# Performance work log

Measured on AMD Instinct MI355X. Metric: run time of the kernel, lower is better.

Reference implementation:

```python
import jax, jax.numpy as jnp
import numpy as np

NEG = -1e30

def setup_inputs() -> dict:
    key = jax.random.key(0)
    ks = jax.random.split(key, 11)
    B, NA, NB = 8, 2048, 2048
    in_A, in_B, out_dim = 256, 256, 64
    s = 0.05
    return {
        "h_A": jax.random.normal(ks[0], (B, NA, in_A), jnp.float32),
        "h_B": jax.random.normal(ks[1], (B, NB, in_B), jnp.float32),
        "mask": jax.random.bernoulli(ks[2], 0.5, (B, NA, NB)),
        "WA_w": jax.random.normal(ks[3], (in_A, out_dim), jnp.float32) * s,
        "WA_b": jax.random.normal(ks[4], (out_dim,), jnp.float32) * s,
        "WB_w": jax.random.normal(ks[5], (in_B, out_dim), jnp.float32) * s,
        "WB_b": jax.random.normal(ks[6], (out_dim,), jnp.float32) * s,
        "aA_w": jax.random.normal(ks[7], (out_dim,), jnp.float32) * s,
        "aA_b": jax.random.normal(ks[8], (), jnp.float32) * s,
        "aB_w": jax.random.normal(ks[9], (out_dim,), jnp.float32) * s,
        "aB_b": jax.random.normal(ks[10], (), jnp.float32) * s,
    }

def reference(h_A, h_B, mask, WA_w, WA_b, WB_w, WB_b, aA_w, aA_b, aB_w, aB_b):
    # Linear projections: z_A [B,NA,D], z_B [B,NB,D]
    z_A = jnp.einsum('bnd,df->bnf', h_A, WA_w) + WA_b
    z_B = jnp.einsum('bmd,df->bmf', h_B, WB_w) + WB_b
    # Additive attention scores: [B,NA,1] + [B,1,NB] -> [B,NA,NB]
    sA = z_A @ aA_w + aA_b  # [B,NA]
    sB = z_B @ aB_w + aB_b  # [B,NB]
    e = sA[:, :, None] + sB[:, None, :]
    e = jnp.where(mask, e, NEG)
    e = jax.nn.leaky_relu(e, negative_slope=0.01)
    alpha = jax.nn.softmax(e, axis=-1)
    alpha = jnp.where(mask, alpha, 0.0)
    # Weighted sum over neighbors
    return jnp.einsum('bnm,bmf->bnf', alpha, z_B)
```

## Files before the change

kernel.cpp:

```cpp
#include <hip/hip_runtime.h>

typedef short bf16x8 __attribute__((ext_vector_type(8)));
typedef float f32x4 __attribute__((ext_vector_type(4)));

__device__ __forceinline__ unsigned short f2bf(float x) {
  unsigned u = __float_as_uint(x);
  u += 0x7FFFu + ((u >> 16) & 1u);
  return (unsigned short)(u >> 16);
}
__device__ __forceinline__ float bf2f(unsigned short h) {
  return __uint_as_float(((unsigned)h) << 16);
}

__global__ __launch_bounds__(256) void zb_kernel(
    const float* __restrict__ hB, const float* __restrict__ WB_w,
    const float* __restrict__ WB_b, const float* __restrict__ aB_w,
    const float* __restrict__ aB_b,
    unsigned short* __restrict__ zBT, float* __restrict__ sB,
    float* __restrict__ msB_blk) {
  __shared__ char wt[32768];
  __shared__ char hl[16384];
  __shared__ float redp[4][16];
  __shared__ float sred[32];

  const int t = threadIdx.x, w = t >> 6, l = t & 63;
  const int q = l >> 4, ln = l & 15;
  const int m0g = blockIdx.x * 32;
  const int b = m0g >> 11, mloc = m0g & 2047;

  {
    const int f = t >> 2, kseg = t & 3;
    #pragma unroll
    for (int j = 0; j < 8; ++j) {
      const int k0 = kseg * 64 + j * 8;
      bf16x8 v;
      #pragma unroll
      for (int jj = 0; jj < 8; ++jj)
        v[jj] = (short)f2bf(WB_w[(k0 + jj) * 64 + f]);
      *(bf16x8*)(wt + ((f * 512 + k0 * 2) ^ ((f & 7) << 4))) = v;
    }
  }
  {
    #pragma unroll
    for (int i = 0; i < 8; ++i) {
      const int idx = i * 1024 + t * 4;
      const int row = idx >> 8, k = idx & 255;
      const float4 x = *(const float4*)(hB + (size_t)m0g * 256 + idx);
      uint2 pk;
      pk.x = (unsigned)f2bf(x.x) | ((unsigned)f2bf(x.y) << 16);
      pk.y = (unsigned)f2bf(x.z) | ((unsigned)f2bf(x.w) << 16);
      *(uint2*)(hl + ((row * 512 + k * 2) ^ ((row & 7) << 4))) = pk;
    }
  }
  __syncthreads();
  const int rt = w & 1, fpair = w >> 1;
  f32x4 acc[2];
  acc[0] = (f32x4){0.f, 0.f, 0.f, 0.f};
  acc[1] = acc[0];
  const int rowA = rt * 16 + ln;
  #pragma unroll
  for (int kk = 0; kk < 8; ++kk) {
    const int ko = kk * 64 + q * 16;
    const bf16x8 a = *(const bf16x8*)(hl + ((rowA * 512 + ko) ^ ((rowA & 7) << 4)));
    #pragma unroll
    for (int j = 0; j < 2; ++j) {
      const int f = fpair * 32 + j * 16 + ln;
      const bf16x8 bb = *(const bf16x8*)(wt + ((f * 512 + ko) ^ ((f & 7) << 4)));
      acc[j] = __builtin_amdgcn_mfma_f32_16x16x32_bf16(a, bb, acc[j], 0, 0, 0);
    }
  }
  float z[2][4];
  float p[4] = {0.f, 0.f, 0.f, 0.f};
  #pragma unroll
  for (int j = 0; j < 2; ++j) {
    const int f = fpair * 32 + j * 16 + ln;
    const float bias = WB_b[f], aw = aB_w[f];
    #pragma unroll
    for (int r = 0; r < 4; ++r) {
      const float zz = acc[j][r] + bias;
      z[j][r] = zz;
      p[r] += zz * aw;
    }
  }
  #pragma unroll
  for (int r = 0; r < 4; ++r) {
    #pragma unroll
    for (int off = 1; off < 16; off <<= 1) p[r] += __shfl_xor(p[r], off, 16);
  }
  if (ln == 0) {
    #pragma unroll
    for (int r = 0; r < 4; ++r) redp[w][q * 4 + r] = p[r];
  }
  __syncthreads();
  char* zt = hl;
  #pragma unroll
  for (int j = 0; j < 2; ++j) {
    const int f = fpair * 32 + j * 16 + ln;
    uint2 pk;
    pk.x = (unsigned)f2bf(z[j][0]) | ((unsigned)f2bf(z[j][1]) << 16);
    pk.y = (unsigned)f2bf(z[j][2]) | ((unsigned)f2bf(z[j][3]) << 16);
    *(uint2*)(zt + f * 80 + (rt * 16 + q * 4) * 2) = pk;
  }
  if (t < 32) {
    const int rtm = t >> 4, mi = t & 15;
    const float s = redp[rtm][mi] + redp[rtm + 2][mi] + aB_b[0];
    sB[m0g + t] = s;
    sred[t] = s;
  }
  __syncthreads();
  if (t == 0) {
    float bm = sred[0];
    #pragma unroll
    for (int i = 1; i < 32; ++i) bm = fmaxf(bm, sred[i]);
    msB_blk[blockIdx.x] = bm;
  }
  {
    const int f = t >> 2, mseg = t & 3;
    const bf16x8 v = *(const bf16x8*)(zt + f * 80 + mseg * 16);
    *(bf16x8*)(zBT + (size_t)b * 131072 + f * 2048 + mloc + mseg * 8) = v;
  }
}

struct Pref {
  bf16x8 za, zb2;
  uint2 mk;
  int4 m32a, m32b;
};

__device__ __forceinline__ void gat_load(Pref& p,
    const unsigned short* zrow, const unsigned char* mk8, const int* mk32,
    const bool use8, const int m0) {
  p.za = *(const bf16x8*)(zrow + m0);
  p.zb2 = *(const bf16x8*)(zrow + m0 + 8);
  if (use8) {
    p.mk = *(const uint2*)(mk8 + m0);
  } else {
    p.m32a = *(const int4*)(mk32 + m0);
    p.m32b = *(const int4*)(mk32 + m0 + 4);
  }
}

__device__ __forceinline__ void gat_body(const Pref& p, char* zc, char* wc,
    const float* sBl, const int m0, const int m8, const float sAr, const float M,
    const bool use8, const int zw0, const int zw1, const int wbyte, float& ds) {
  *(bf16x8*)(zc + zw0) = p.za;
  *(bf16x8*)(zc + zw1) = p.zb2;
  const int sbase = m0 + m8 * 8;
  const float4 s0 = *(const float4*)(sBl + sbase);
  const float4 s1 = *(const float4*)(sBl + sbase + 4);
  const float sbx[8] = {s0.x, s0.y, s0.z, s0.w, s1.x, s1.y, s1.z, s1.w};
  int km[8];
  if (use8) {
    #pragma unroll
    for (int j = 0; j < 4; ++j) {
      km[j] = (p.mk.x >> (8 * j)) & 0xFF;
      km[j + 4] = (p.mk.y >> (8 * j)) & 0xFF;
    }
  } else {
    km[0] = p.m32a.x; km[1] = p.m32a.y; km[2] = p.m32a.z; km[3] = p.m32a.w;
    km[4] = p.m32b.x; km[5] = p.m32b.y; km[6] = p.m32b.z; km[7] = p.m32b.w;
  }
  unsigned short wb[8];
  #pragma unroll
  for (int j = 0; j < 8; ++j) {
    const float x = sAr + sbx[j];
    const float e = x >= 0.f ? x : 0.01f * x;
    const float v = km[j] ? __expf(e - M) : 0.f;
    wb[j] = f2bf(v);
    ds += bf2f(wb[j]);
  }
  uint4 pk;
  pk.x = (unsigned)wb[0] | ((unsigned)wb[1] << 16);
  pk.y = (unsigned)wb[2] | ((unsigned)wb[3] << 16);
  pk.z = (unsigned)wb[4] | ((unsigned)wb[5] << 16);
  pk.w = (unsigned)wb[6] | ((unsigned)wb[7] << 16);
  *(uint4*)(wc + wbyte) = pk;
}

__device__ __forceinline__ void gat_mfma(const char* zc, const char* wc,
    f32x4& acc, const int fb, const int ar, const int q) {
  #pragma unroll
  for (int kk = 0; kk < 4; ++kk) {
    const int ko = kk * 64 + q * 16;
    const bf16x8 bb = *(const bf16x8*)(zc + ((fb * 256 + ko) ^ ((fb & 7) << 4)));
    const bf16x8 aa = *(const bf16x8*)(wc + ((ar * 256 + ko) ^ ((ar & 7) << 4)));
    acc = __builtin_amdgcn_mfma_f32_16x16x32_bf16(aa, bb, acc, 0, 0, 0);
  }
}

__global__ __launch_bounds__(512, 4) void gat_kernel(
    const unsigned short* __restrict__ zBT, const float* __restrict__ hA,
    const float* __restrict__ WA_w, const float* __restrict__ WA_b,
    const float* __restrict__ aA_w, const float* __restrict__ aA_b,
    const float* __restrict__ sB, const float* __restrict__ msB_blk,
    const unsigned char* __restrict__ mask8, const int* __restrict__ mask32,
    float* __restrict__ out) {
  const int b = blockIdx.y, n0 = blockIdx.x * 32;
  const int t = threadIdx.x, w = t >> 6, l = t & 63;
  const int q = l >> 4, ln = l & 15;

  __shared__ char zbl0[16384], zbl1[16384];
  __shared__ char wl0[8192], wl1[8192];
  __shared__ float sBl[2048];
  __shared__ float vAl[256];
  __shared__ float sAl[32];
  __shared__ float dl[32];
  __shared__ float cAl;
  __shared__ unsigned dfl[4];

  if (t < 256) {
    const unsigned vdet = mask8[t * 4 + 1];
    const unsigned long long bal = __ballot(vdet != 0);
    if (l == 0) dfl[w] = (bal != 0ull) ? 1u : 0u;
    const float4* wr = (const float4*)(WA_w + t * 64);
    const float4* a4 = (const float4*)aA_w;
    float s = 0.f;
    #pragma unroll
    for (int i = 0; i < 16; ++i) {
      const float4 x = wr[i], y = a4[i];
      s += x.x * y.x + x.y * y.y + x.z * y.z + x.w * y.w;
    }
    vAl[t] = s;
  } else {
    const int u = t - 256;
    ((float4*)sBl)[u * 2] = ((const float4*)(sB + b * 2048))[u * 2];
    ((float4*)sBl)[u * 2 + 1] = ((const float4*)(sB + b * 2048))[u * 2 + 1];
    if (u == 0) {
      float ca = aA_b[0];
      for (int f = 0; f < 64; ++f) ca += WA_b[f] * aA_w[f];
      cAl = ca;
    }
  }
  float mb = msB_blk[b * 64 + l];
  #pragma unroll
  for (int off = 1; off < 64; off <<= 1) mb = fmaxf(mb, __shfl_xor(mb, off, 64));
  __syncthreads();
  const bool use8 = (dfl[0] | dfl[1] | dfl[2] | dfl[3]) != 0;
  {
    const float4 vA4 = ((const float4*)vAl)[l];
    const float cA0 = cAl;
    #pragma unroll
    for (int rr = 0; rr < 4; ++rr) {
      const int row = w * 4 + rr;
      const float4 h4 = *(const float4*)(hA + ((size_t)(b * 2048 + n0 + row)) * 256 + l * 4);
      float s = h4.x * vA4.x + h4.y * vA4.y + h4.z * vA4.z + h4.w * vA4.w;
      #pragma unroll
      for (int off = 1; off < 64; off <<= 1) s += __shfl_xor(s, off, 64);
      if (l == 0) sAl[row] = s + cA0;
    }
  }
  __syncthreads();

  const int r = t >> 4, m8 = t & 15;
  const float sAr = sAl[r];
  const float Mf = sAr + mb;
  const float M = Mf >= 0.f ? Mf : 0.01f * Mf;
  float ds = 0.f;
  f32x4 acc = (f32x4){0.f, 0.f, 0.f, 0.f};

  const int zf = t >> 3, zseg = t & 7;
  const unsigned short* zrow = zBT + (size_t)b * 131072 + zf * 2048 + zseg * 16;
  const size_t mrowe = ((size_t)(b * 2048 + n0 + r)) * 2048 + m8 * 8;
  const unsigned char* mk8 = mask8 + mrowe;
  const int* mk32 = mask32 + mrowe;
  const int zbase = zf * 256 + zseg * 32;
  const int swz = (zf & 7) << 4;
  const int zw0 = zbase ^ swz, zw1 = (zbase + 16) ^ swz;
  const int wbyte = (r * 256 + m8 * 16) ^ ((r & 7) << 4);
  const int fb = (w >> 1) * 16 + ln;
  const int ar = (w & 1) * 16 + ln;

  Pref pA, pB;
  gat_load(pA, zrow, mk8, mk32, use8, 0);
  for (int mt = 0; mt < 16; mt += 2) {
    gat_load(pB, zrow, mk8, mk32, use8, (mt + 1) * 128);
    gat_body(pA, zbl0, wl0, sBl, mt * 128, m8, sAr, M, use8, zw0, zw1, wbyte, ds);
    __syncthreads();
    gat_mfma(zbl0, wl0, acc, fb, ar, q);
    gat_load(pA, zrow, mk8, mk32, use8, ((mt + 2) & 15) * 128);
    gat_body(pB, zbl1, wl1, sBl, (mt + 1) * 128, m8, sAr, M, use8, zw0, zw1, wbyte, ds);
    __syncthreads();
    gat_mfma(zbl1, wl1, acc, fb, ar, q);
  }
  #pragma unroll
  for (int off = 1; off < 16; off <<= 1) ds += __shfl_xor(ds, off, 16);
  if (m8 == 0) dl[r] = ds;
  __syncthreads();
  #pragma unroll
  for (int rr = 0; rr < 4; ++rr) {
    const int n = (w & 1) * 16 + q * 4 + rr;
    const float d = dl[n];
    out[((size_t)(b * 2048 + n0 + n)) * 64 + fb] = d > 0.f ? acc[rr] / d : 0.f;
  }
}

extern "C" void kernel_launch(void* const* d_in, const int* in_sizes, int n_in,
                              void* d_out, int out_size, void* d_ws, size_t ws_size,
                              hipStream_t stream) {
  const float* h_A = (const float*)d_in[0];
  const float* h_B = (const float*)d_in[1];
  const unsigned char* mask8 = (const unsigned char*)d_in[2];
  const int* mask32 = (const int*)d_in[2];
  const float* WA_w = (const float*)d_in[3];
  const float* WA_b = (const float*)d_in[4];
  const float* WB_w = (const float*)d_in[5];
  const float* WB_b = (const float*)d_in[6];
  const float* aA_w = (const float*)d_in[7];
  const float* aA_b = (const float*)d_in[8];
  const float* aB_w = (const float*)d_in[9];
  const float* aB_b = (const float*)d_in[10];
  float* out = (float*)d_out;

  char* wsb = (char*)d_ws;
  unsigned short* zBT = (unsigned short*)wsb;
  float* sB      = (float*)(wsb + 2097152);
  float* msB_blk = (float*)(wsb + 2162688);

  zb_kernel<<<512, 256, 0, stream>>>(h_B, WB_w, WB_b, aB_w, aB_b, zBT, sB, msB_blk);
  gat_kernel<<<dim3(64, 8), 512, 0, stream>>>(zBT, h_A, WA_w, WA_b, aA_w, aA_b,
                                              sB, msB_blk, mask8, mask32, out);
}
```

Measured before the change: 59.30 us.

## Double rows per block and switch to 32x32x16 MFMA with split-K merge

Each block now handles 64 query rows instead of 32, so every staged zB tile in shared memory is reused by twice as many rows, halving zB reloads. The matmul moves from 16x16x32 to 32x32x16 MFMA, with the two wave halves splitting K and merging partial sums through shared memory at the end. The int32 mask path is packed into bytes at load time. Cost: grid drops to 256 blocks (one wave on a 256-CU part), and each thread does twice the exp work and holds more registers, so occupancy and latency hiding may suffer.

```diff
diff --git a/kernel.cpp b/kernel.cpp
--- a/kernel.cpp
+++ b/kernel.cpp
@@ -2,6 +2,7 @@
 
 typedef short bf16x8 __attribute__((ext_vector_type(8)));
 typedef float f32x4 __attribute__((ext_vector_type(4)));
+typedef float f32x16 __attribute__((ext_vector_type(16)));
 
 __device__ __forceinline__ unsigned short f2bf(float x) {
   unsigned u = __float_as_uint(x);
@@ -123,68 +124,80 @@
 
 struct Pref {
   bf16x8 za, zb2;
-  uint2 mk;
-  int4 m32a, m32b;
+  uint2 mk0, mk1;
 };
 
-__device__ __forceinline__ void gat_load(Pref& p,
-    const unsigned short* zrow, const unsigned char* mk8, const int* mk32,
-    const bool use8, const int m0) {
+__device__ __forceinline__ uint2 pack_mask32(const int* p) {
+  const int4 a = *(const int4*)p;
+  const int4 c = *(const int4*)(p + 4);
+  uint2 r;
+  r.x = (a.x ? 1u : 0u) | (a.y ? 0x100u : 0u) | (a.z ? 0x10000u : 0u) | (a.w ? 0x1000000u : 0u);
+  r.y = (c.x ? 1u : 0u) | (c.y ? 0x100u : 0u) | (c.z ? 0x10000u : 0u) | (c.w ? 0x1000000u : 0u);
+  return r;
+}
+
+__device__ __forceinline__ void gat_load(Pref& p, const unsigned short* zrow,
+    const unsigned char* mk8a, const unsigned char* mk8b,
+    const int* mk32a, const int* mk32b, const bool use8, const int m0) {
   p.za = *(const bf16x8*)(zrow + m0);
   p.zb2 = *(const bf16x8*)(zrow + m0 + 8);
   if (use8) {
-    p.mk = *(const uint2*)(mk8 + m0);
+    p.mk0 = *(const uint2*)(mk8a + m0);
+    p.mk1 = *(const uint2*)(mk8b + m0);
   } else {
-    p.m32a = *(const int4*)(mk32 + m0);
-    p.m32b = *(const int4*)(mk32 + m0 + 4);
+    p.mk0 = pack_mask32(mk32a + m0);
+    p.mk1 = pack_mask32(mk32b + m0);
   }
 }
 
 __device__ __forceinline__ void gat_body(const Pref& p, char* zc, char* wc,
-    const float* sBl, const int m0, const int m8, const float sAr, const float M,
-    const bool use8, const int zw0, const int zw1, const int wbyte, float& ds) {
+    const float* sBl, const int m0, const int m8,
+    const float sA0, const float sA1, const float M0, const float M1,
+    const int zw0, const int zw1, const int wbyte0, float& ds0, float& ds1) {
   *(bf16x8*)(zc + zw0) = p.za;
   *(bf16x8*)(zc + zw1) = p.zb2;
   const int sbase = m0 + m8 * 8;
   const float4 s0 = *(const float4*)(sBl + sbase);
   const float4 s1 = *(const float4*)(sBl + sbase + 4);
   const float sbx[8] = {s0.x, s0.y, s0.z, s0.w, s1.x, s1.y, s1.z, s1.w};
-  int km[8];
-  if (use8) {
-    #pragma unroll
-    for (int j = 0; j < 4; ++j) {
-      km[j] = (p.mk.x >> (8 * j)) & 0xFF;
-      km[j + 4] = (p.mk.y >> (8 * j)) & 0xFF;
-    }
-  } else {
-    km[0] = p.m32a.x; km[1] = p.m32a.y; km[2] = p.m32a.z; km[3] = p.m32a.w;
-    km[4] = p.m32b.x; km[5] = p.m32b.y; km[6] = p.m32b.z; km[7] = p.m32b.w;
-  }
-  unsigned short wb[8];
+  unsigned km0[8], km1[8];
+  #pragma unroll
+  for (int j = 0; j < 4; ++j) {
+    km0[j] = (p.mk0.x >> (8 * j)) & 0xFFu; km0[j + 4] = (p.mk0.y >> (8 * j)) & 0xFFu;
+    km1[j] = (p.mk1.x >> (8 * j)) & 0xFFu; km1[j + 4] = (p.mk1.y >> (8 * j)) & 0xFFu;
+  }
+  unsigned short w0[8], w1[8];
   #pragma unroll
   for (int j = 0; j < 8; ++j) {
-    const float x = sAr + sbx[j];
-    const float e = x >= 0.f ? x : 0.01f * x;
-    const float v = km[j] ? __expf(e - M) : 0.f;
-    wb[j] = f2bf(v);
-    ds += bf2f(wb[j]);
-  }
-  uint4 pk;
-  pk.x = (unsigned)wb[0] | ((unsigned)wb[1] << 16);
-  pk.y = (unsigned)wb[2] | ((unsigned)wb[3] << 16);
-  pk.z = (unsigned)wb[4] | ((unsigned)wb[5] << 16);
-  pk.w = (unsigned)wb[6] | ((unsigned)wb[7] << 16);
-  *(uint4*)(wc + wbyte) = pk;
+    const float x0 = sA0 + sbx[j];
+    const float e0 = x0 >= 0.f ? x0 : 0.01f * x0;
+    const float v0 = km0[j] ? __expf(e0 - M0) : 0.f;
+    w0[j] = f2bf(v0); ds0 += bf2f(w0[j]);
+    const float x1 = sA1 + sbx[j];
+    const float e1 = x1 >= 0.f ? x1 : 0.01f * x1;
+    const float v1 = km1[j] ? __expf(e1 - M1) : 0.f;
+    w1[j] = f2bf(v1); ds1 += bf2f(w1[j]);
+  }
+  uint4 pk0, pk1;
+  pk0.x = (unsigned)w0[0] | ((unsigned)w0[1] << 16);
+  pk0.y = (unsigned)w0[2] | ((unsigned)w0[3] << 16);
+  pk0.z = (unsigned)w0[4] | ((unsigned)w0[5] << 16);
+  pk0.w = (unsigned)w0[6] | ((unsigned)w0[7] << 16);
+  pk1.x = (unsigned)w1[0] | ((unsigned)w1[1] << 16);
+  pk1.y = (unsigned)w1[2] | ((unsigned)w1[3] << 16);
+  pk1.z = (unsigned)w1[4] | ((unsigned)w1[5] << 16);
+  pk1.w = (unsigned)w1[6] | ((unsigned)w1[7] << 16);
+  *(uint4*)(wc + wbyte0) = pk0;
+  *(uint4*)(wc + wbyte0 + 8192) = pk1;
 }
 
 __device__ __forceinline__ void gat_mfma(const char* zc, const char* wc,
-    f32x4& acc, const int fb, const int ar, const int q) {
-  #pragma unroll
-  for (int kk = 0; kk < 4; ++kk) {
-    const int ko = kk * 64 + q * 16;
-    const bf16x8 bb = *(const bf16x8*)(zc + ((fb * 256 + ko) ^ ((fb & 7) << 4)));
-    const bf16x8 aa = *(const bf16x8*)(wc + ((ar * 256 + ko) ^ ((ar & 7) << 4)));
-    acc = __builtin_amdgcn_mfma_f32_16x16x32_bf16(aa, bb, acc, 0, 0, 0);
+    f32x16& acc, const int abase, const int aswz, const int bbase, const int bswz) {
+  #pragma unroll
+  for (int ks = 0; ks < 4; ++ks) {
+    const bf16x8 aa = *(const bf16x8*)(wc + ((abase + ks * 32) ^ aswz));
+    const bf16x8 bb = *(const bf16x8*)(zc + ((bbase + ks * 32) ^ bswz));
+    acc = __builtin_amdgcn_mfma_f32_32x32x16_bf16(aa, bb, acc, 0, 0, 0);
   }
 }
 
@@ -195,16 +208,15 @@
     const float* __restrict__ sB, const float* __restrict__ msB_blk,
     const unsigned char* __restrict__ mask8, const int* __restrict__ mask32,
     float* __restrict__ out) {
-  const int b = blockIdx.y, n0 = blockIdx.x * 32;
+  const int b = blockIdx.y, n0 = blockIdx.x * 64;
   const int t = threadIdx.x, w = t >> 6, l = t & 63;
-  const int q = l >> 4, ln = l & 15;
 
   __shared__ char zbl0[16384], zbl1[16384];
-  __shared__ char wl0[8192], wl1[8192];
+  __shared__ char wl0[16384], wl1[16384];
   __shared__ float sBl[2048];
   __shared__ float vAl[256];
-  __shared__ float sAl[32];
-  __shared__ float dl[32];
+  __shared__ float sAl[64];
+  __shared__ float dl[64];
   __shared__ float cAl;
   __shared__ unsigned dfl[4];
 
@@ -212,9 +224,9 @@
     const unsigned vdet = mask8[t * 4 + 1];
     const unsigned long long bal = __ballot(vdet != 0);
     if (l == 0) dfl[w] = (bal != 0ull) ? 1u : 0u;
+    float s = 0.f;
     const float4* wr = (const float4*)(WA_w + t * 64);
     const float4* a4 = (const float4*)aA_w;
-    float s = 0.f;
     #pragma unroll
     for (int i = 0; i < 16; ++i) {
       const float4 x = wr[i], y = a4[i];
@@ -240,8 +252,8 @@
     const float4 vA4 = ((const float4*)vAl)[l];
     const float cA0 = cAl;
     #pragma unroll
-    for (int rr = 0; rr < 4; ++rr) {
-      const int row = w * 4 + rr;
+    for (int rr = 0; rr < 8; ++rr) {
+      const int row = w * 8 + rr;
       const float4 h4 = *(const float4*)(hA + ((size_t)(b * 2048 + n0 + row)) * 256 + l * 4);
       float s = h4.x * vA4.x + h4.y * vA4.y + h4.z * vA4.z + h4.w * vA4.w;
       #pragma unroll
@@ -251,46 +263,75 @@
   }
   __syncthreads();
 
-  const int r = t >> 4, m8 = t & 15;
-  const float sAr = sAl[r];
-  const float Mf = sAr + mb;
-  const float M = Mf >= 0.f ? Mf : 0.01f * Mf;
-  float ds = 0.f;
-  f32x4 acc = (f32x4){0.f, 0.f, 0.f, 0.f};
+  const int r0 = t >> 4, m8 = t & 15;
+  const float sA0 = sAl[r0], sA1 = sAl[r0 + 32];
+  const float M0f = sA0 + mb, M1f = sA1 + mb;
+  const float M0 = M0f >= 0.f ? M0f : 0.01f * M0f;
+  const float M1 = M1f >= 0.f ? M1f : 0.01f * M1f;
+  float ds0 = 0.f, ds1 = 0.f;
+  f32x16 acc;
+  #pragma unroll
+  for (int i = 0; i < 16; ++i) acc[i] = 0.f;
 
   const int zf = t >> 3, zseg = t & 7;
   const unsigned short* zrow = zBT + (size_t)b * 131072 + zf * 2048 + zseg * 16;
-  const size_t mrowe = ((size_t)(b * 2048 + n0 + r)) * 2048 + m8 * 8;
-  const unsigned char* mk8 = mask8 + mrowe;
-  const int* mk32 = mask32 + mrowe;
-  const int zbase = zf * 256 + zseg * 32;
-  const int swz = (zf & 7) << 4;
-  const int zw0 = zbase ^ swz, zw1 = (zbase + 16) ^ swz;
-  const int wbyte = (r * 256 + m8 * 16) ^ ((r & 7) << 4);
-  const int fb = (w >> 1) * 16 + ln;
-  const int ar = (w & 1) * 16 + ln;
+  const int zswz = (zf & 15) << 4;
+  const int zw0 = (zf * 256 + zseg * 32) ^ zswz;
+  const int zw1 = (zf * 256 + zseg * 32 + 16) ^ zswz;
+  const size_t mrow0 = ((size_t)(b * 2048 + n0 + r0)) * 2048 + m8 * 8;
+  const size_t mrow1 = mrow0 + (size_t)32 * 2048;
+  const unsigned char* mk8a = mask8 + mrow0;
+  const unsigned char* mk8b = mask8 + mrow1;
+  const int* mk32a = mask32 + mrow0;
+  const int* mk32b = mask32 + mrow1;
+  const int wbyte0 = (r0 * 256 + m8 * 16) ^ ((r0 & 15) << 4);
+  const int wn = w & 1, wf = (w >> 1) & 1, wm = w >> 2;
+  const int arow = wn * 32 + (l & 31);
+  const int brow = wf * 32 + (l & 31);
+  const int abase = arow * 256 + wm * 128 + (l >> 5) * 16;
+  const int bbase = brow * 256 + wm * 128 + (l >> 5) * 16;
+  const int aswz = (arow & 15) << 4;
+  const int bswz = (brow & 15) << 4;
 
   Pref pA, pB;
-  gat_load(pA, zrow, mk8, mk32, use8, 0);
+  gat_load(pA, zrow, mk8a, mk8b, mk32a, mk32b, use8, 0);
   for (int mt = 0; mt < 16; mt += 2) {
-    gat_load(pB, zrow, mk8, mk32, use8, (mt + 1) * 128);
-    gat_body(pA, zbl0, wl0, sBl, mt * 128, m8, sAr, M, use8, zw0, zw1, wbyte, ds);
+    gat_load(pB, zrow, mk8a, mk8b, mk32a, mk32b, use8, (mt + 1) * 128);
+    gat_body(pA, zbl0, wl0, sBl, mt * 128, m8, sA0, sA1, M0, M1, zw0, zw1, wbyte0, ds0, ds1);
     __syncthreads();
-    gat_mfma(zbl0, wl0, acc, fb, ar, q);
-    gat_load(pA, zrow, mk8, mk32, use8, ((mt + 2) & 15) * 128);
-    gat_body(pB, zbl1, wl1, sBl, (mt + 1) * 128, m8, sAr, M, use8, zw0, zw1, wbyte, ds);
+    gat_mfma(zbl0, wl0, acc, abase, aswz, bbase, bswz);
+    gat_load(pA, zrow, mk8a, mk8b, mk32a, mk32b, use8, ((mt + 2) & 15) * 128);
+    gat_body(pB, zbl1, wl1, sBl, (mt + 1) * 128, m8, sA0, sA1, M0, M1, zw0, zw1, wbyte0, ds0, ds1);
     __syncthreads();
-    gat_mfma(zbl1, wl1, acc, fb, ar, q);
-  }
-  #pragma unroll
-  for (int off = 1; off < 16; off <<= 1) ds += __shfl_xor(ds, off, 16);
-  if (m8 == 0) dl[r] = ds;
-  __syncthreads();
-  #pragma unroll
-  for (int rr = 0; rr < 4; ++rr) {
-    const int n = (w & 1) * 16 + q * 4 + rr;
-    const float d = dl[n];
-    out[((size_t)(b * 2048 + n0 + n)) * 64 + fb] = d > 0.f ? acc[rr] / d : 0.f;
+    gat_mfma(zbl1, wl1, acc, abase, aswz, bbase, bswz);
+  }
+
+  #pragma unroll
+  for (int off = 1; off < 16; off <<= 1) {
+    ds0 += __shfl_xor(ds0, off, 16);
+    ds1 += __shfl_xor(ds1, off, 16);
+  }
+  if (m8 == 0) { dl[r0] = ds0; dl[r0 + 32] = ds1; }
+  __syncthreads();
+  float* mrg = (float*)zbl0;
+  const int quad = (wn * 2 + wf) * 1024;
+  if (wm == 1) {
+    #pragma unroll
+    for (int r = 0; r < 16; ++r) {
+      const int row = (r & 3) + 8 * (r >> 2) + 4 * (l >> 5);
+      mrg[quad + row * 32 + (l & 31)] = acc[r];
+    }
+  }
+  __syncthreads();
+  if (wm == 0) {
+    #pragma unroll
+    for (int r = 0; r < 16; ++r) {
+      const int row = (r & 3) + 8 * (r >> 2) + 4 * (l >> 5);
+      const float v = acc[r] + mrg[quad + row * 32 + (l & 31)];
+      const int n = wn * 32 + row;
+      const float d = dl[n];
+      out[((size_t)(b * 2048 + n0 + n)) * 64 + wf * 32 + (l & 31)] = d > 0.f ? v / d : 0.f;
+    }
   }
 }
 
@@ -317,6 +358,6 @@
   float* msB_blk = (float*)(wsb + 2162688);
 
   zb_kernel<<<512, 256, 0, stream>>>(h_B, WB_w, WB_b, aB_w, aB_b, zBT, sB, msB_blk);
-  gat_kernel<<<dim3(64, 8), 512, 0, stream>>>(zBT, h_A, WA_w, WA_b, aA_w, aA_b,
+  gat_kernel<<<dim3(32, 8), 512, 0, stream>>>(zBT, h_A, WA_w, WA_b, aA_w, aA_b,
                                               sB, msB_blk, mask8, mask32, out);
 }
```

After: 60.81 us. +2.5%, slower.

## Split attention over neighbor quarters, keep operands in registers, add merge kernel

Applied to the files above, without the earlier changes.

The attention kernel now splits the neighbor dimension into four chunks across a third grid axis and writes partial weighted sums and denominators, which a new merge kernel adds up and normalizes. The per-row sA projection moves into the zB kernel. The main loop feeds MFMAs directly from registers: weights are built in-register as the A operand and z_B is loaded straight from global memory as B operands, so the shared-memory staging and per-iteration barriers are gone. The cost is about 17 MB of extra partial-result traffic, a third kernel launch, and more redundant global z_B loads per block.

```diff
diff --git a/kernel.cpp b/kernel.cpp
--- a/kernel.cpp
+++ b/kernel.cpp
@@ -8,25 +8,55 @@
   u += 0x7FFFu + ((u >> 16) & 1u);
   return (unsigned short)(u >> 16);
 }
-__device__ __forceinline__ float bf2f(unsigned short h) {
-  return __uint_as_float(((unsigned)h) << 16);
-}
 
 __global__ __launch_bounds__(256) void zb_kernel(
     const float* __restrict__ hB, const float* __restrict__ WB_w,
     const float* __restrict__ WB_b, const float* __restrict__ aB_w,
     const float* __restrict__ aB_b,
+    const float* __restrict__ hA, const float* __restrict__ WA_w,
+    const float* __restrict__ WA_b, const float* __restrict__ aA_w,
+    const float* __restrict__ aA_b,
     unsigned short* __restrict__ zBT, float* __restrict__ sB,
-    float* __restrict__ msB_blk) {
+    float* __restrict__ msB_blk, float* __restrict__ sA) {
   __shared__ char wt[32768];
   __shared__ char hl[16384];
   __shared__ float redp[4][16];
   __shared__ float sred[32];
+  __shared__ float vAl[256];
+  __shared__ float cAl;
 
   const int t = threadIdx.x, w = t >> 6, l = t & 63;
   const int q = l >> 4, ln = l & 15;
   const int m0g = blockIdx.x * 32;
   const int b = m0g >> 11, mloc = m0g & 2047;
+
+  {
+    float sa = 0.f;
+    const float4* wr4 = (const float4*)(WA_w + t * 64);
+    const float4* aa4 = (const float4*)aA_w;
+    #pragma unroll
+    for (int i = 0; i < 16; ++i) {
+      const float4 x = wr4[i], y = aa4[i];
+      sa += x.x * y.x + x.y * y.y + x.z * y.z + x.w * y.w;
+    }
+    vAl[t] = sa;
+    if (t == 0) {
+      float ca = aA_b[0];
+      for (int f = 0; f < 64; ++f) ca += WA_b[f] * aA_w[f];
+      cAl = ca;
+    }
+    __syncthreads();
+    const float4 v4 = ((const float4*)vAl)[l];
+    #pragma unroll
+    for (int rr = 0; rr < 8; ++rr) {
+      const int row = w * 8 + rr;
+      const float4 h4 = *(const float4*)(hA + (size_t)(m0g + row) * 256 + l * 4);
+      float s = h4.x * v4.x + h4.y * v4.y + h4.z * v4.z + h4.w * v4.w;
+      #pragma unroll
+      for (int off = 1; off < 64; off <<= 1) s += __shfl_xor(s, off, 64);
+      if (l == 0) sA[m0g + row] = s + cAl;
+    }
+  }
 
   {
     const int f = t >> 2, kseg = t & 3;
@@ -122,176 +152,131 @@
 }
 
 struct Pref {
-  bf16x8 za, zb2;
   uint2 mk;
-  int4 m32a, m32b;
+  bf16x8 z0, z1, z2, z3;
 };
 
-__device__ __forceinline__ void gat_load(Pref& p,
-    const unsigned short* zrow, const unsigned char* mk8, const int* mk32,
-    const bool use8, const int m0) {
-  p.za = *(const bf16x8*)(zrow + m0);
-  p.zb2 = *(const bf16x8*)(zrow + m0 + 8);
-  if (use8) {
-    p.mk = *(const uint2*)(mk8 + m0);
-  } else {
-    p.m32a = *(const int4*)(mk32 + m0);
-    p.m32b = *(const int4*)(mk32 + m0 + 4);
-  }
-}
-
-__device__ __forceinline__ void gat_body(const Pref& p, char* zc, char* wc,
-    const float* sBl, const int m0, const int m8, const float sAr, const float M,
-    const bool use8, const int zw0, const int zw1, const int wbyte, float& ds) {
-  *(bf16x8*)(zc + zw0) = p.za;
-  *(bf16x8*)(zc + zw1) = p.zb2;
-  const int sbase = m0 + m8 * 8;
-  const float4 s0 = *(const float4*)(sBl + sbase);
-  const float4 s1 = *(const float4*)(sBl + sbase + 4);
-  const float sbx[8] = {s0.x, s0.y, s0.z, s0.w, s1.x, s1.y, s1.z, s1.w};
-  int km[8];
-  if (use8) {
-    #pragma unroll
-    for (int j = 0; j < 4; ++j) {
-      km[j] = (p.mk.x >> (8 * j)) & 0xFF;
-      km[j + 4] = (p.mk.y >> (8 * j)) & 0xFF;
-    }
-  } else {
-    km[0] = p.m32a.x; km[1] = p.m32a.y; km[2] = p.m32a.z; km[3] = p.m32a.w;
-    km[4] = p.m32b.x; km[5] = p.m32b.y; km[6] = p.m32b.z; km[7] = p.m32b.w;
-  }
-  unsigned short wb[8];
+__device__ __forceinline__ uint2 pack_mask32(const int* p) {
+  const int4 a = *(const int4*)p;
+  const int4 c = *(const int4*)(p + 4);
+  uint2 r;
+  r.x = (a.x ? 1u : 0u) | (a.y ? 0x100u : 0u) | (a.z ? 0x10000u : 0u) | (a.w ? 0x1000000u : 0u);
+  r.y = (c.x ? 1u : 0u) | (c.y ? 0x100u : 0u) | (c.z ? 0x10000u : 0u) | (c.w ? 0x1000000u : 0u);
+  return r;
+}
+
+__device__ __forceinline__ void gat_load(Pref& p, const unsigned char* mp8,
+    const int* mp32, const unsigned short* zp0, const unsigned short* zp1,
+    const unsigned short* zp2, const unsigned short* zp3,
+    const bool use8, const int c) {
+  const int m = (c & 15) * 32;
+  if (use8) p.mk = *(const uint2*)(mp8 + m);
+  else p.mk = pack_mask32(mp32 + m);
+  p.z0 = *(const bf16x8*)(zp0 + m);
+  p.z1 = *(const bf16x8*)(zp1 + m);
+  p.z2 = *(const bf16x8*)(zp2 + m);
+  p.z3 = *(const bf16x8*)(zp3 + m);
+}
+
+__device__ __forceinline__ void gat_compute(const Pref& p, const float* sBl,
+    const int c, const int lq8, const float sAr, const float M,
+    f32x4& a0, f32x4& a1, f32x4& a2, f32x4& a3, float& ds) {
+  const int sb0 = c * 32 + lq8;
+  const float4 s0 = *(const float4*)(sBl + sb0);
+  const float4 s1 = *(const float4*)(sBl + sb0 + 4);
+  const float sx[8] = {s0.x, s0.y, s0.z, s0.w, s1.x, s1.y, s1.z, s1.w};
+  bf16x8 af;
   #pragma unroll
   for (int j = 0; j < 8; ++j) {
-    const float x = sAr + sbx[j];
-    const float e = x >= 0.f ? x : 0.01f * x;
-    const float v = km[j] ? __expf(e - M) : 0.f;
-    wb[j] = f2bf(v);
-    ds += bf2f(wb[j]);
-  }
-  uint4 pk;
-  pk.x = (unsigned)wb[0] | ((unsigned)wb[1] << 16);
-  pk.y = (unsigned)wb[2] | ((unsigned)wb[3] << 16);
-  pk.z = (unsigned)wb[4] | ((unsigned)wb[5] << 16);
-  pk.w = (unsigned)wb[6] | ((unsigned)wb[7] << 16);
-  *(uint4*)(wc + wbyte) = pk;
-}
-
-__device__ __forceinline__ void gat_mfma(const char* zc, const char* wc,
-    f32x4& acc, const int fb, const int ar, const int q) {
-  #pragma unroll
-  for (int kk = 0; kk < 4; ++kk) {
-    const int ko = kk * 64 + q * 16;
-    const bf16x8 bb = *(const bf16x8*)(zc + ((fb * 256 + ko) ^ ((fb & 7) << 4)));
-    const bf16x8 aa = *(const bf16x8*)(wc + ((ar * 256 + ko) ^ ((ar & 7) << 4)));
-    acc = __builtin_amdgcn_mfma_f32_16x16x32_bf16(aa, bb, acc, 0, 0, 0);
-  }
-}
-
-__global__ __launch_bounds__(512, 4) void gat_kernel(
-    const unsigned short* __restrict__ zBT, const float* __restrict__ hA,
-    const float* __restrict__ WA_w, const float* __restrict__ WA_b,
-    const float* __restrict__ aA_w, const float* __restrict__ aA_b,
+    const unsigned km = ((j < 4 ? p.mk.x : p.mk.y) >> (8 * (j & 3))) & 0xFFu;
+    const float x = sAr + sx[j];
+    const float e = fmaxf(x, 0.01f * x);
+    const float v = km ? __expf(e - M) : 0.f;
+    af[j] = (short)f2bf(v);
+    ds += v;
+  }
+  a0 = __builtin_amdgcn_mfma_f32_16x16x32_bf16(af, p.z0, a0, 0, 0, 0);
+  a1 = __builtin_amdgcn_mfma_f32_16x16x32_bf16(af, p.z1, a1, 0, 0, 0);
+  a2 = __builtin_amdgcn_mfma_f32_16x16x32_bf16(af, p.z2, a2, 0, 0, 0);
+  a3 = __builtin_amdgcn_mfma_f32_16x16x32_bf16(af, p.z3, a3, 0, 0, 0);
+}
+
+__global__ __launch_bounds__(256, 4) void gat_kernel(
+    const unsigned short* __restrict__ zBT, const float* __restrict__ sA,
     const float* __restrict__ sB, const float* __restrict__ msB_blk,
     const unsigned char* __restrict__ mask8, const int* __restrict__ mask32,
-    float* __restrict__ out) {
-  const int b = blockIdx.y, n0 = blockIdx.x * 32;
+    float* __restrict__ pacc, float* __restrict__ pd) {
+  const int b = blockIdx.y, n0 = blockIdx.x * 64, mq = blockIdx.z;
   const int t = threadIdx.x, w = t >> 6, l = t & 63;
-  const int q = l >> 4, ln = l & 15;
-
-  __shared__ char zbl0[16384], zbl1[16384];
-  __shared__ char wl0[8192], wl1[8192];
-  __shared__ float sBl[2048];
-  __shared__ float vAl[256];
-  __shared__ float sAl[32];
-  __shared__ float dl[32];
-  __shared__ float cAl;
+  const int ln = l & 15, lq = l >> 4, lq8 = lq * 8;
+
+  __shared__ float sBl[512];
   __shared__ unsigned dfl[4];
 
-  if (t < 256) {
-    const unsigned vdet = mask8[t * 4 + 1];
-    const unsigned long long bal = __ballot(vdet != 0);
-    if (l == 0) dfl[w] = (bal != 0ull) ? 1u : 0u;
-    const float4* wr = (const float4*)(WA_w + t * 64);
-    const float4* a4 = (const float4*)aA_w;
-    float s = 0.f;
-    #pragma unroll
-    for (int i = 0; i < 16; ++i) {
-      const float4 x = wr[i], y = a4[i];
-      s += x.x * y.x + x.y * y.y + x.z * y.z + x.w * y.w;
-    }
-    vAl[t] = s;
-  } else {
-    const int u = t - 256;
-    ((float4*)sBl)[u * 2] = ((const float4*)(sB + b * 2048))[u * 2];
-    ((float4*)sBl)[u * 2 + 1] = ((const float4*)(sB + b * 2048))[u * 2 + 1];
-    if (u == 0) {
-      float ca = aA_b[0];
-      for (int f = 0; f < 64; ++f) ca += WA_b[f] * aA_w[f];
-      cAl = ca;
-    }
-  }
+  const unsigned vdet = mask8[t * 4 + 1];
+  const unsigned long long bal = __ballot(vdet != 0);
+  if (l == 0) dfl[w] = (bal != 0ull) ? 1u : 0u;
+  ((float2*)sBl)[t] = ((const float2*)(sB + b * 2048 + mq * 512))[t];
   float mb = msB_blk[b * 64 + l];
   #pragma unroll
   for (int off = 1; off < 64; off <<= 1) mb = fmaxf(mb, __shfl_xor(mb, off, 64));
   __syncthreads();
   const bool use8 = (dfl[0] | dfl[1] | dfl[2] | dfl[3]) != 0;
-  {
-    const float4 vA4 = ((const float4*)vAl)[l];
-    const float cA0 = cAl;
-    #pragma unroll
-    for (int rr = 0; rr < 4; ++rr) {
-      const int row = w * 4 + rr;
-      const float4 h4 = *(const float4*)(hA + ((size_t)(b * 2048 + n0 + row)) * 256 + l * 4);
-      float s = h4.x * vA4.x + h4.y * vA4.y + h4.z * vA4.z + h4.w * vA4.w;
-      #pragma unroll
-      for (int off = 1; off < 64; off <<= 1) s += __shfl_xor(s, off, 64);
-      if (l == 0) sAl[row] = s + cA0;
-    }
-  }
-  __syncthreads();
-
-  const int r = t >> 4, m8 = t & 15;
-  const float sAr = sAl[r];
+
+  const int row = n0 + w * 16 + ln;
+  const float sAr = sA[b * 2048 + row];
   const float Mf = sAr + mb;
-  const float M = Mf >= 0.f ? Mf : 0.01f * Mf;
+  const float M = fmaxf(Mf, 0.01f * Mf);
   float ds = 0.f;
-  f32x4 acc = (f32x4){0.f, 0.f, 0.f, 0.f};
-
-  const int zf = t >> 3, zseg = t & 7;
-  const unsigned short* zrow = zBT + (size_t)b * 131072 + zf * 2048 + zseg * 16;
-  const size_t mrowe = ((size_t)(b * 2048 + n0 + r)) * 2048 + m8 * 8;
-  const unsigned char* mk8 = mask8 + mrowe;
-  const int* mk32 = mask32 + mrowe;
-  const int zbase = zf * 256 + zseg * 32;
-  const int swz = (zf & 7) << 4;
-  const int zw0 = zbase ^ swz, zw1 = (zbase + 16) ^ swz;
-  const int wbyte = (r * 256 + m8 * 16) ^ ((r & 7) << 4);
-  const int fb = (w >> 1) * 16 + ln;
-  const int ar = (w & 1) * 16 + ln;
+  f32x4 a0 = (f32x4){0.f, 0.f, 0.f, 0.f}, a1 = a0, a2 = a0, a3 = a0;
+
+  const size_t mbase = ((size_t)(b * 2048 + row)) * 2048 + mq * 512 + lq8;
+  const unsigned char* mp8 = mask8 + mbase;
+  const int* mp32 = mask32 + mbase;
+  const unsigned short* zp0 = zBT + ((size_t)(b * 64 + ln)) * 2048 + mq * 512 + lq8;
+  const unsigned short* zp1 = zp0 + 16 * 2048;
+  const unsigned short* zp2 = zp0 + 32 * 2048;
+  const unsigned short* zp3 = zp0 + 48 * 2048;
 
   Pref pA, pB;
-  gat_load(pA, zrow, mk8, mk32, use8, 0);
-  for (int mt = 0; mt < 16; mt += 2) {
-    gat_load(pB, zrow, mk8, mk32, use8, (mt + 1) * 128);
-    gat_body(pA, zbl0, wl0, sBl, mt * 128, m8, sAr, M, use8, zw0, zw1, wbyte, ds);
-    __syncthreads();
-    gat_mfma(zbl0, wl0, acc, fb, ar, q);
-    gat_load(pA, zrow, mk8, mk32, use8, ((mt + 2) & 15) * 128);
-    gat_body(pB, zbl1, wl1, sBl, (mt + 1) * 128, m8, sAr, M, use8, zw0, zw1, wbyte, ds);
-    __syncthreads();
-    gat_mfma(zbl1, wl1, acc, fb, ar, q);
-  }
-  #pragma unroll
-  for (int off = 1; off < 16; off <<= 1) ds += __shfl_xor(ds, off, 16);
-  if (m8 == 0) dl[r] = ds;
-  __syncthreads();
-  #pragma unroll
-  for (int rr = 0; rr < 4; ++rr) {
-    const int n = (w & 1) * 16 + q * 4 + rr;
-    const float d = dl[n];
-    out[((size_t)(b * 2048 + n0 + n)) * 64 + fb] = d > 0.f ? acc[rr] / d : 0.f;
-  }
+  gat_load(pA, mp8, mp32, zp0, zp1, zp2, zp3, use8, 0);
+  for (int c = 0; c < 16; c += 2) {
+    gat_load(pB, mp8, mp32, zp0, zp1, zp2, zp3, use8, c + 1);
+    gat_compute(pA, sBl, c, lq8, sAr, M, a0, a1, a2, a3, ds);
+    gat_load(pA, mp8, mp32, zp0, zp1, zp2, zp3, use8, c + 2);
+    gat_compute(pB, sBl, c + 1, lq8, sAr, M, a0, a1, a2, a3, ds);
+  }
+
+  ds += __shfl_xor(ds, 16, 64);
+  ds += __shfl_xor(ds, 32, 64);
+  if (l < 16) pd[(size_t)(mq * 8 + b) * 2048 + n0 + w * 16 + l] = ds;
+  const size_t obase = ((size_t)(mq * 8 + b) * 2048 + n0 + w * 16 + lq * 4) * 64 + ln;
+  #pragma unroll
+  for (int r = 0; r < 4; ++r) {
+    float* o = pacc + obase + (size_t)r * 64;
+    o[0] = a0[r];
+    o[16] = a1[r];
+    o[32] = a2[r];
+    o[48] = a3[r];
+  }
+}
+
+__global__ __launch_bounds__(256) void merge_kernel(
+    const float* __restrict__ pacc, const float* __restrict__ pd,
+    float* __restrict__ out) {
+  const int tid = blockIdx.x * 256 + threadIdx.x;
+  const int bn = tid >> 4;
+  const float4* p4 = (const float4*)pacc;
+  const float4 x0 = p4[tid], x1 = p4[262144 + tid];
+  const float4 x2 = p4[524288 + tid], x3 = p4[786432 + tid];
+  const float d = pd[bn] + pd[16384 + bn] + pd[32768 + bn] + pd[49152 + bn];
+  const float inv = d > 0.f ? 1.f / d : 0.f;
+  float4 o;
+  o.x = (x0.x + x1.x + x2.x + x3.x) * inv;
+  o.y = (x0.y + x1.y + x2.y + x3.y) * inv;
+  o.z = (x0.z + x1.z + x2.z + x3.z) * inv;
+  o.w = (x0.w + x1.w + x2.w + x3.w) * inv;
+  ((float4*)out)[tid] = o;
 }
 
 extern "C" void kernel_launch(void* const* d_in, const int* in_sizes, int n_in,
@@ -314,9 +299,15 @@
   char* wsb = (char*)d_ws;
   unsigned short* zBT = (unsigned short*)wsb;
   float* sB      = (float*)(wsb + 2097152);
-  float* msB_blk = (float*)(wsb + 2162688);
-
-  zb_kernel<<<512, 256, 0, stream>>>(h_B, WB_w, WB_b, aB_w, aB_b, zBT, sB, msB_blk);
-  gat_kernel<<<dim3(64, 8), 512, 0, stream>>>(zBT, h_A, WA_w, WA_b, aA_w, aA_b,
-                                              sB, msB_blk, mask8, mask32, out);
-}
+  float* sA      = (float*)(wsb + 2162688);
+  float* msB_blk = (float*)(wsb + 2228224);
+  float* pacc    = (float*)(wsb + 2230272);
+  float* pd      = (float*)(wsb + 19007488);
+
+  zb_kernel<<<512, 256, 0, stream>>>(h_B, WB_w, WB_b, aB_w, aB_b,
+                                     h_A, WA_w, WA_b, aA_w, aA_b,
+                                     zBT, sB, msB_blk, sA);
+  gat_kernel<<<dim3(32, 8, 4), 256, 0, stream>>>(zBT, sA, sB, msB_blk,
+                                                 mask8, mask32, pacc, pd);
+  merge_kernel<<<1024, 256, 0, stream>>>(pacc, pd, out);
+}
```

Result: slower. 74.85 us (+26.2%).
